# Performance work log

Measured on AMD Instinct MI355X. Metric: run time of the kernel, lower is better.

The kernel has to match this reference:

```python
import jax, jax.numpy as jnp
import numpy as np

B, N = 8192, 32          # batch of (user,item) pairs, AOS triples per pair
D1, D2 = 64, 64          # user/item and aspect/opinion embedding dims
H, O = 128, 64           # hidden_dims = [128, 64]
R = 3                    # n_relations (sentiments)
SLOPE = 0.01             # nn.LeakyReLU default negative_slope


def leaky_relu(x):
    return jnp.where(x >= 0, x, SLOPE * x)


def setup_inputs() -> dict:
    key = jax.random.key(0)
    ks = jax.random.split(key, 14)
    p = 0.1  # param scale
    return {
        "u_emb": jax.random.normal(ks[0], (B, D1), jnp.float32),
        "i_emb": jax.random.normal(ks[1], (B, D1), jnp.float32),
        "a_emb": jax.random.normal(ks[2], (B, N, D2), jnp.float32),
        "o_emb": jax.random.normal(ks[3], (B, N, D2), jnp.float32),
        "s": jax.random.randint(ks[4], (B, N), 0, R, jnp.int64),
        # per-relation AO MLP: Linear(128->128) + LeakyReLU, Linear(128->64) + LeakyReLU
        "ao_W0": jax.random.normal(ks[5], (R, 2 * D2, H), jnp.float32) * p,
        "ao_b0": jax.random.normal(ks[6], (R, H), jnp.float32) * p,
        "ao_W1": jax.random.normal(ks[7], (R, H, O), jnp.float32) * p,
        "ao_b1": jax.random.normal(ks[8], (R, O), jnp.float32) * p,
        # shared UI MLP: Linear(128->128) + LeakyReLU, Linear(128->64) + LeakyReLU
        "ui_W0": jax.random.normal(ks[9], (2 * D1, H), jnp.float32) * p,
        "ui_b0": jax.random.normal(ks[10], (H,), jnp.float32) * p,
        "ui_W1": jax.random.normal(ks[11], (H, O), jnp.float32) * p,
        "ui_b1": jax.random.normal(ks[12], (O,), jnp.float32) * p,
    }


def reference(u_emb, i_emb, a_emb, o_emb, s,
              ao_W0, ao_b0, ao_W1, ao_b1,
              ui_W0, ui_b0, ui_W1, ui_b1):
    # ui branch (shared MLP)
    ui_in = jnp.concatenate([u_emb, i_emb], axis=-1)            # [B, 2*D1]
    ui = leaky_relu(ui_in @ ui_W0 + ui_b0)                       # [B, H]
    ui = leaky_relu(ui @ ui_W1 + ui_b1)                          # [B, O]

    # ao branch: relation-specific MLPs. Instead of masked gather/scatter,
    # compute all R (small) relation MLPs densely and select per element.
    ao_in = jnp.concatenate([a_emb, o_emb], axis=-1)             # [B, N, 2*D2]
    h = leaky_relu(jnp.einsum('bnd,rdh->rbnh', ao_in, ao_W0)
                   + ao_b0[:, None, None, :])                    # [R, B, N, H]
    h = leaky_relu(jnp.einsum('rbnh,rho->rbno', h, ao_W1)
                   + ao_b1[:, None, None, :])                    # [R, B, N, O]

    h = jnp.moveaxis(h, 0, 2)                                    # [B, N, R, O]
    aos = jnp.take_along_axis(h, s[:, :, None, None], axis=2)[:, :, 0, :]  # [B, N, O]

    # loss == 'bpr': dot product score
    pred = jnp.sum(ui[:, None, :] * aos, axis=-1)                # [B, N]
    return pred
```

## Files before the change

kernel.cpp:

```cpp
#include <hip/hip_runtime.h>

typedef unsigned short u16t;
typedef __bf16 bf16x8 __attribute__((ext_vector_type(8)));
typedef float  f32x4  __attribute__((ext_vector_type(4)));

#define SLOPE 0.01f
#define SAP 136
#define UIP 72

__device__ __forceinline__ float lrelu(float x) { return x >= 0.0f ? x : SLOPE * x; }
__device__ __forceinline__ u16t f2b(float f) {
    union { float f; unsigned i; } x; x.f = f;
    return (u16t)((x.i + 0x7fffu + ((x.i >> 16) & 1u)) >> 16);
}
__device__ __forceinline__ float b2f(u16t u) {
    union { unsigned i; float f; } x; x.i = ((unsigned)u) << 16; return x.f;
}
__device__ __forceinline__ unsigned pk2(float a, float b) {
    unsigned r;
    asm("v_cvt_pk_bf16_f32 %0, %1, %2" : "=v"(r) : "v"(a), "v"(b));
    return r;
}
__device__ __forceinline__ uint4 pack8(float4 x, float4 y) {
    uint4 r; r.x = pk2(x.x, x.y); r.y = pk2(x.z, x.w);
    r.z = pk2(y.x, y.y); r.w = pk2(y.z, y.w); return r;
}
__device__ __forceinline__ int clmp3(int v) { return v < 0 ? 0 : (v > 2 ? 2 : v); }

__global__ __launch_bounds__(256) void kernelA(
    const float* __restrict__ W0, const float* __restrict__ W1,
    const float* __restrict__ uW0, const float* __restrict__ uW1,
    const int* __restrict__ s,
    u16t* __restrict__ W0p, u16t* __restrict__ W1p,
    u16t* __restrict__ U0p, u16t* __restrict__ U1p,
    int* __restrict__ cntB)
{
    __shared__ int sc[3];
    const int t = threadIdx.x;
    if (blockIdx.x < 384) {
        int tid = blockIdx.x * 256 + t;
        if (tid < 49152) {
            int j = tid & 7, lane = (tid >> 3) & 63, c = (tid >> 9) & 7,
                kk = (tid >> 12) & 3, r = tid >> 14;
            int k = kk * 32 + (lane >> 4) * 8 + j, n = c * 16 + (lane & 15);
            W0p[tid] = f2b(W0[(r * 128 + k) * 128 + n]);
        } else if (tid < 73728) {
            int t2 = tid - 49152;
            int j = t2 & 7, lane = (t2 >> 3) & 63, c = (t2 >> 9) & 3,
                kk = (t2 >> 11) & 3, r = t2 >> 13;
            int k = kk * 32 + (lane >> 4) * 8 + j, n = c * 16 + (lane & 15);
            W1p[t2] = f2b(W1[(r * 128 + k) * 64 + n]);
        } else if (tid < 90112) {
            int t3 = tid - 73728;
            int j = t3 & 7, lane = (t3 >> 3) & 63, c = (t3 >> 9) & 7, kk = t3 >> 12;
            int k = kk * 32 + (lane >> 4) * 8 + j, n = c * 16 + (lane & 15);
            U0p[t3] = f2b(uW0[k * 128 + n]);
        } else if (tid < 98304) {
            int t4 = tid - 90112;
            int j = t4 & 7, lane = (t4 >> 3) & 63, c = (t4 >> 9) & 3, kk = t4 >> 11;
            int k = kk * 32 + (lane >> 4) * 8 + j, n = c * 16 + (lane & 15);
            U1p[t4] = f2b(uW1[k * 64 + n]);
        }
    } else {
        const int blk = blockIdx.x - 384;
        if (t < 3) sc[t] = 0;
        __syncthreads();
        int4 sv = ((const int4*)s)[blk * 256 + t];
        int l0 = 0, l1 = 0, l2 = 0, r;
        r = clmp3(sv.x); l0 += (r == 0); l1 += (r == 1); l2 += (r == 2);
        r = clmp3(sv.y); l0 += (r == 0); l1 += (r == 1); l2 += (r == 2);
        r = clmp3(sv.z); l0 += (r == 0); l1 += (r == 1); l2 += (r == 2);
        r = clmp3(sv.w); l0 += (r == 0); l1 += (r == 1); l2 += (r == 2);
        atomicAdd(&sc[0], l0); atomicAdd(&sc[1], l1); atomicAdd(&sc[2], l2);
        __syncthreads();
        if (t < 3) cntB[blk * 3 + t] = sc[t];
    }
}

__global__ __launch_bounds__(512) void kernelB(
    const float* __restrict__ u_emb, const float* __restrict__ i_emb,
    const u16t* __restrict__ U0p, const u16t* __restrict__ U1p,
    const float* __restrict__ uib0, const float* __restrict__ uib1,
    const int* __restrict__ s, const int* __restrict__ cntB,
    u16t* __restrict__ uiT, int* __restrict__ cntOut, int* __restrict__ rows)
{
    __shared__ __align__(16) u16t sA[32 * SAP];
    __shared__ __align__(16) u16t sH[32 * SAP];
    __shared__ int sTab[768];
    __shared__ int sBT[6];
    __shared__ int sS[256];
    const int t = threadIdx.x;

    if (blockIdx.x < 256) {
        const int wave = t >> 6, lane = t & 63, m = lane & 15, kg = lane >> 4;
        const int c = wave, c2 = wave & 3, hlf = wave >> 2;
        const int B0 = blockIdx.x * 32;

        bf16x8 w0f[4], w1f[4];
#pragma unroll
        for (int kk = 0; kk < 4; ++kk) {
            w0f[kk] = *(const bf16x8*)(U0p + (((kk * 8 + c) * 64 + lane) << 3));
            w1f[kk] = *(const bf16x8*)(U1p + (((kk * 4 + c2) * 64 + lane) << 3));
        }
        const float b0 = uib0[c * 16 + m], b1 = uib1[c2 * 16 + m];

        {
            const int row = t >> 4, seg = t & 15;
            const float* src = (seg < 8) ? (u_emb + (size_t)(B0 + row) * 64 + seg * 8)
                                         : (i_emb + (size_t)(B0 + row) * 64 + (seg - 8) * 8);
            float4 v0 = ((const float4*)src)[0], v1 = ((const float4*)src)[1];
            *(uint4*)&sA[row * SAP + seg * 8] = pack8(v0, v1);
        }
        __syncthreads();

#pragma unroll
        for (int mt = 0; mt < 2; ++mt) {
            const u16t* ap = &sA[(mt * 16 + m) * SAP + kg * 8];
            bf16x8 a0 = *(const bf16x8*)(ap),      a1 = *(const bf16x8*)(ap + 32);
            bf16x8 a2 = *(const bf16x8*)(ap + 64), a3 = *(const bf16x8*)(ap + 96);
            f32x4 acc = {0.f, 0.f, 0.f, 0.f};
            acc = __builtin_amdgcn_mfma_f32_16x16x32_bf16(a0, w0f[0], acc, 0, 0, 0);
            acc = __builtin_amdgcn_mfma_f32_16x16x32_bf16(a1, w0f[1], acc, 0, 0, 0);
            acc = __builtin_amdgcn_mfma_f32_16x16x32_bf16(a2, w0f[2], acc, 0, 0, 0);
            acc = __builtin_amdgcn_mfma_f32_16x16x32_bf16(a3, w0f[3], acc, 0, 0, 0);
#pragma unroll
            for (int j = 0; j < 4; ++j)
                sH[(mt * 16 + kg * 4 + j) * SAP + c * 16 + m] = f2b(lrelu(acc[j] + b0));
        }
        __syncthreads();

        {
            const int mt = hlf;
            const u16t* hp = &sH[(mt * 16 + m) * SAP + kg * 8];
            bf16x8 a0 = *(const bf16x8*)(hp),      a1 = *(const bf16x8*)(hp + 32);
            bf16x8 a2 = *(const bf16x8*)(hp + 64), a3 = *(const bf16x8*)(hp + 96);
            f32x4 acc = {0.f, 0.f, 0.f, 0.f};
            acc = __builtin_amdgcn_mfma_f32_16x16x32_bf16(a0, w1f[0], acc, 0, 0, 0);
            acc = __builtin_amdgcn_mfma_f32_16x16x32_bf16(a1, w1f[1], acc, 0, 0, 0);
            acc = __builtin_amdgcn_mfma_f32_16x16x32_bf16(a2, w1f[2], acc, 0, 0, 0);
            acc = __builtin_amdgcn_mfma_f32_16x16x32_bf16(a3, w1f[3], acc, 0, 0, 0);
#pragma unroll
            for (int j = 0; j < 4; ++j)
                uiT[(size_t)(B0 + mt * 16 + kg * 4 + j) * 64 + c2 * 16 + m] =
                    f2b(lrelu(acc[j] + b1));
        }
    } else {
        const int blk = blockIdx.x - 256;
        if (t < 256) {
            sTab[t] = cntB[t]; sTab[t + 256] = cntB[t + 256]; sTab[t + 512] = cntB[t + 512];
        }
        __syncthreads();
        if (t < 3) {
            int base = 0, tot = 0;
            for (int b = 0; b < 256; ++b) {
                int v = sTab[b * 3 + t];
                if (b < blk) base += v;
                tot += v;
            }
            sBT[t] = base; sBT[3 + t] = tot;
        }
        int rr0 = 0, rr1 = 0, rr2 = 0, rr3 = 0, packed = 0;
        if (t < 256) {
            int4 sv = ((const int4*)s)[blk * 256 + t];
            rr0 = clmp3(sv.x); rr1 = clmp3(sv.y); rr2 = clmp3(sv.z); rr3 = clmp3(sv.w);
            packed = (1 << (11 * rr0)) + (1 << (11 * rr1))
                   + (1 << (11 * rr2)) + (1 << (11 * rr3));
            sS[t] = packed;
        }
        __syncthreads();
        for (int off = 1; off < 256; off <<= 1) {
            int v = 0;
            if (t >= off && t < 256) v = sS[t - off];
            __syncthreads();
            if (t < 256) sS[t] += v;
            __syncthreads();
        }
        if (t < 256) {
            const int excl = sS[t] - packed;
            const int g1 = sBT[3], g2 = sBT[3] + sBT[4];
            int rr[4] = { rr0, rr1, rr2, rr3 };
            int seen[3] = {0, 0, 0};
#pragma unroll
            for (int i = 0; i < 4; ++i) {
                int rl = rr[i];
                int gb = rl == 0 ? 0 : (rl == 1 ? g1 : g2);
                int pos = gb + sBT[rl] + ((excl >> (11 * rl)) & 2047) + seen[rl];
                seen[rl]++;
                rows[pos] = blk * 1024 + t * 4 + i;
            }
        }
        if (blk == 0 && t < 3) cntOut[t] = sBT[3 + t];
    }
}

__global__ __launch_bounds__(512, 4) void ao_main(
    const float* __restrict__ a_emb, const float* __restrict__ o_emb,
    const float* __restrict__ ao_b0, const float* __restrict__ ao_b1,
    const u16t* __restrict__ W0p, const u16t* __restrict__ W1p,
    const u16t* __restrict__ uiT, const int* __restrict__ rows,
    const int* __restrict__ tot, float* __restrict__ out)
{
    __shared__ __align__(16) u16t sA[64 * SAP];
    __shared__ __align__(16) u16t sH[64 * SAP];
    __shared__ __align__(16) u16t sUIl[64 * UIP];
    __shared__ float sPred[64];

    const int n0 = tot[0], n1 = tot[1], n2 = tot[2];
    const int ch0 = (n0 + 63) >> 6, ch1 = (n1 + 63) >> 6, ch2 = (n2 + 63) >> 6;
    const int nch = ch0 + ch1 + ch2;

    const int t = threadIdx.x, wave = t >> 6, lane = t & 63, m = lane & 15, kg = lane >> 4;
    const int c = wave, c2 = wave & 3, hlf = wave >> 2;

    bf16x8 w0f[4], w1f[4];
    float b0 = 0.f, b1 = 0.f;
    int rprev = -1;

    for (int ci = 0; ci < 2; ++ci) {
        const int chunk = blockIdx.x * 2 + ci;
        if (chunk >= nch) break;
        int r, rel, bb, nb;
        if (chunk < ch0)            { r = 0; rel = chunk;             bb = 0;       nb = n0; }
        else if (chunk < ch0 + ch1) { r = 1; rel = chunk - ch0;       bb = n0;      nb = n1; }
        else                        { r = 2; rel = chunk - ch0 - ch1; bb = n0 + n1; nb = n2; }
        const int rstart = rel * 64;
        int nrows = nb - rstart; if (nrows > 64) nrows = 64;

        if (r != rprev) {
            const u16t* wp0 = W0p + r * 16384;
            const u16t* wp1 = W1p + r * 8192;
#pragma unroll
            for (int kk = 0; kk < 4; ++kk) {
                w0f[kk] = *(const bf16x8*)(wp0 + (((kk * 8 + c) * 64 + lane) << 3));
                w1f[kk] = *(const bf16x8*)(wp1 + (((kk * 4 + c2) * 64 + lane) << 3));
            }
            b0 = ao_b0[r * 128 + c * 16 + m];
            b1 = ao_b1[r * 64 + c2 * 16 + m];
            rprev = r;
        }

        {
            const int q = t >> 3, seg = t & 7;
            const int rid = rows[bb + rstart + (q < nrows ? q : nrows - 1)];
            const float* src = (seg < 4) ? (a_emb + (size_t)rid * 64 + seg * 16)
                                         : (o_emb + (size_t)rid * 64 + (seg - 4) * 16);
            float4 v0 = ((const float4*)src)[0], v1 = ((const float4*)src)[1];
            float4 v2 = ((const float4*)src)[2], v3 = ((const float4*)src)[3];
            uint4* dst = (uint4*)&sA[q * SAP + seg * 16];
            dst[0] = pack8(v0, v1);
            dst[1] = pack8(v2, v3);
            *(uint4*)&sUIl[q * UIP + seg * 8] =
                *(const uint4*)(uiT + ((size_t)(rid >> 5)) * 64 + seg * 8);
        }
        if (t < 64) sPred[t] = 0.0f;
        __syncthreads();

#pragma unroll
        for (int mt = 0; mt < 4; ++mt) {
            const u16t* ap = &sA[(mt * 16 + m) * SAP + kg * 8];
            bf16x8 a0 = *(const bf16x8*)(ap),      a1 = *(const bf16x8*)(ap + 32);
            bf16x8 a2 = *(const bf16x8*)(ap + 64), a3 = *(const bf16x8*)(ap + 96);
            f32x4 acc_a = {0.f, 0.f, 0.f, 0.f}, acc_b = {0.f, 0.f, 0.f, 0.f};
            acc_a = __builtin_amdgcn_mfma_f32_16x16x32_bf16(a0, w0f[0], acc_a, 0, 0, 0);
            acc_a = __builtin_amdgcn_mfma_f32_16x16x32_bf16(a1, w0f[1], acc_a, 0, 0, 0);
            acc_b = __builtin_amdgcn_mfma_f32_16x16x32_bf16(a2, w0f[2], acc_b, 0, 0, 0);
            acc_b = __builtin_amdgcn_mfma_f32_16x16x32_bf16(a3, w0f[3], acc_b, 0, 0, 0);
            f32x4 acc = acc_a + acc_b;
#pragma unroll
            for (int j = 0; j < 4; ++j)
                sH[(mt * 16 + kg * 4 + j) * SAP + c * 16 + m] = f2b(lrelu(acc[j] + b0));
        }
        __syncthreads();

        for (int mt = hlf; mt < 4; mt += 2) {
            const u16t* hp = &sH[(mt * 16 + m) * SAP + kg * 8];
            bf16x8 a0 = *(const bf16x8*)(hp),      a1 = *(const bf16x8*)(hp + 32);
            bf16x8 a2 = *(const bf16x8*)(hp + 64), a3 = *(const bf16x8*)(hp + 96);
            f32x4 acc_a = {0.f, 0.f, 0.f, 0.f}, acc_b = {0.f, 0.f, 0.f, 0.f};
            acc_a = __builtin_amdgcn_mfma_f32_16x16x32_bf16(a0, w1f[0], acc_a, 0, 0, 0);
            acc_a = __builtin_amdgcn_mfma_f32_16x16x32_bf16(a1, w1f[1], acc_a, 0, 0, 0);
            acc_b = __builtin_amdgcn_mfma_f32_16x16x32_bf16(a2, w1f[2], acc_b, 0, 0, 0);
            acc_b = __builtin_amdgcn_mfma_f32_16x16x32_bf16(a3, w1f[3], acc_b, 0, 0, 0);
            f32x4 acc = acc_a + acc_b;
            const int o = c2 * 16 + m;
            float pj[4];
#pragma unroll
            for (int j = 0; j < 4; ++j) {
                const int q = mt * 16 + kg * 4 + j;
                pj[j] = lrelu(acc[j] + b1) * b2f(sUIl[q * UIP + o]);
            }
#pragma unroll
            for (int msk = 8; msk >= 1; msk >>= 1) {
#pragma unroll
                for (int j = 0; j < 4; ++j) pj[j] += __shfl_xor(pj[j], msk, 16);
            }
            if (m == 0) {
#pragma unroll
                for (int j = 0; j < 4; ++j)
                    atomicAdd(&sPred[mt * 16 + kg * 4 + j], pj[j]);
            }
        }
        __syncthreads();

        if (t < nrows) out[rows[bb + rstart + t]] = sPred[t];
    }
}

extern "C" void kernel_launch(void* const* d_in, const int* in_sizes, int n_in,
                              void* d_out, int out_size, void* d_ws, size_t ws_size,
                              hipStream_t stream) {
    (void)in_sizes; (void)n_in; (void)out_size; (void)ws_size;
    const float* u_emb = (const float*)d_in[0];
    const float* i_emb = (const float*)d_in[1];
    const float* a_emb = (const float*)d_in[2];
    const float* o_emb = (const float*)d_in[3];
    const int*   s     = (const int*)  d_in[4];
    const float* aoW0  = (const float*)d_in[5];
    const float* aob0  = (const float*)d_in[6];
    const float* aoW1  = (const float*)d_in[7];
    const float* aob1  = (const float*)d_in[8];
    const float* uiW0  = (const float*)d_in[9];
    const float* uib0  = (const float*)d_in[10];
    const float* uiW1  = (const float*)d_in[11];
    const float* uib1  = (const float*)d_in[12];
    float* out = (float*)d_out;

    char* ws = (char*)d_ws;
    u16t* W0p  = (u16t*)(ws);
    u16t* W1p  = (u16t*)(ws + 98304);
    u16t* U0p  = (u16t*)(ws + 147456);
    u16t* U1p  = (u16t*)(ws + 180224);
    u16t* uiT  = (u16t*)(ws + 196608);
    int*  cntB = (int*) (ws + 1245184);
    int*  totC = (int*) (ws + 1248256);
    int*  rowsP= (int*) (ws + 1248272);

    kernelA<<<dim3(640), dim3(256), 0, stream>>>(
        aoW0, aoW1, uiW0, uiW1, s, W0p, W1p, U0p, U1p, cntB);
    kernelB<<<dim3(512), dim3(512), 0, stream>>>(
        u_emb, i_emb, U0p, U1p, uib0, uib1, s, cntB, uiT, totC, rowsP);
    ao_main<<<dim3(2051), dim3(512), 0, stream>>>(
        a_emb, o_emb, aob0, aob1, W0p, W1p, uiT, rowsP, totC, out);
}
```

Before: 199.9 us.

## Software-pipeline gathers across chunks with double-buffered UI tiles and fewer barriers

The ao_main kernel now handles four 64-row chunks per block instead of two, and the grid is halved. While the current chunk's MFMAs run, it prefetches the next chunk's a/o embeddings and UI vectors into registers and looks up row indices two chunks ahead. The UI tile and prediction buffers are double-buffered, and each output write is deferred to the following iteration, which cuts the barriers per chunk from three to two. This is meant to hide global gather latency behind compute, at the cost of more register pressure and fewer blocks to balance load across the GPU.

```diff
diff --git a/kernel.cpp b/kernel.cpp
--- a/kernel.cpp
+++ b/kernel.cpp
@@ -7,6 +7,7 @@
 #define SLOPE 0.01f
 #define SAP 136
 #define UIP 72
+#define CPB 4
 
 __device__ __forceinline__ float lrelu(float x) { return x >= 0.0f ? x : SLOPE * x; }
 __device__ __forceinline__ u16t f2b(float f) {
@@ -26,6 +27,12 @@
     r.z = pk2(y.x, y.y); r.w = pk2(y.z, y.w); return r;
 }
 __device__ __forceinline__ int clmp3(int v) { return v < 0 ? 0 : (v > 2 ? 2 : v); }
+
+__device__ __forceinline__ void block_sync() {
+    asm volatile("s_waitcnt lgkmcnt(0)" ::: "memory");
+    __builtin_amdgcn_s_barrier();
+    asm volatile("" ::: "memory");
+}
 
 __global__ __launch_bounds__(256) void kernelA(
     const float* __restrict__ W0, const float* __restrict__ W1,
@@ -193,6 +200,18 @@
     }
 }
 
+__device__ __forceinline__ void chunk_info(int chunk, int ch0, int ch01,
+                                           int n0, int n1, int n2,
+                                           int& r, int& bb, int& rstart, int& nrows)
+{
+    int rel, nb;
+    if (chunk < ch0)       { r = 0; rel = chunk;        bb = 0;       nb = n0; }
+    else if (chunk < ch01) { r = 1; rel = chunk - ch0;  bb = n0;      nb = n1; }
+    else                   { r = 2; rel = chunk - ch01; bb = n0 + n1; nb = n2; }
+    rstart = rel * 64;
+    int nr = nb - rstart; nrows = nr > 64 ? 64 : nr;
+}
+
 __global__ __launch_bounds__(512, 4) void ao_main(
     const float* __restrict__ a_emb, const float* __restrict__ o_emb,
     const float* __restrict__ ao_b0, const float* __restrict__ ao_b1,
@@ -202,29 +221,55 @@
 {
     __shared__ __align__(16) u16t sA[64 * SAP];
     __shared__ __align__(16) u16t sH[64 * SAP];
-    __shared__ __align__(16) u16t sUIl[64 * UIP];
-    __shared__ float sPred[64];
+    __shared__ __align__(16) u16t sUIl[2][64 * UIP];
+    __shared__ float sPred[2][64];
 
     const int n0 = tot[0], n1 = tot[1], n2 = tot[2];
     const int ch0 = (n0 + 63) >> 6, ch1 = (n1 + 63) >> 6, ch2 = (n2 + 63) >> 6;
-    const int nch = ch0 + ch1 + ch2;
+    const int ch01 = ch0 + ch1;
+    const int nch = ch01 + ch2;
+    const int chunk0 = blockIdx.x * CPB;
+    if (chunk0 >= nch) return;
 
     const int t = threadIdx.x, wave = t >> 6, lane = t & 63, m = lane & 15, kg = lane >> 4;
     const int c = wave, c2 = wave & 3, hlf = wave >> 2;
+    const int q = t >> 3, seg = t & 7;
 
     bf16x8 w0f[4], w1f[4];
     float b0 = 0.f, b1 = 0.f;
     int rprev = -1;
 
-    for (int ci = 0; ci < 2; ++ci) {
-        const int chunk = blockIdx.x * 2 + ci;
+    int r0, bb0, rs0, nr0;
+    chunk_info(chunk0, ch0, ch01, n0, n1, n2, r0, bb0, rs0, nr0);
+    int ridCur = rows[bb0 + rs0 + (q < nr0 ? q : nr0 - 1)];
+
+    float4 pv0, pv1, pv2, pv3; uint4 puv;
+    {
+        const float* src = (seg < 4) ? (a_emb + (size_t)ridCur * 64 + seg * 16)
+                                     : (o_emb + (size_t)ridCur * 64 + (seg - 4) * 16);
+        pv0 = ((const float4*)src)[0]; pv1 = ((const float4*)src)[1];
+        pv2 = ((const float4*)src)[2]; pv3 = ((const float4*)src)[3];
+        puv = *(const uint4*)(uiT + ((size_t)(ridCur >> 5)) * 64 + seg * 8);
+    }
+    int ridNext = 0;
+    if (CPB > 1 && chunk0 + 1 < nch) {
+        int r1, bb1, rs1, nr1;
+        chunk_info(chunk0 + 1, ch0, ch01, n0, n1, n2, r1, bb1, rs1, nr1);
+        ridNext = rows[bb1 + rs1 + (q < nr1 ? q : nr1 - 1)];
+    }
+    {
+        uint4* dst = (uint4*)&sA[q * SAP + seg * 16];
+        dst[0] = pack8(pv0, pv1); dst[1] = pack8(pv2, pv3);
+        *(uint4*)&sUIl[0][q * UIP + seg * 8] = puv;
+    }
+    int ridPrev = 0, nrowsPrev = 0, lastPar = 0;
+    block_sync();
+
+    for (int ci = 0; ci < CPB; ++ci) {
+        const int chunk = chunk0 + ci;
         if (chunk >= nch) break;
-        int r, rel, bb, nb;
-        if (chunk < ch0)            { r = 0; rel = chunk;             bb = 0;       nb = n0; }
-        else if (chunk < ch0 + ch1) { r = 1; rel = chunk - ch0;       bb = n0;      nb = n1; }
-        else                        { r = 2; rel = chunk - ch0 - ch1; bb = n0 + n1; nb = n2; }
-        const int rstart = rel * 64;
-        int nrows = nb - rstart; if (nrows > 64) nrows = 64;
+        int r, bb, rstart, nrows;
+        chunk_info(chunk, ch0, ch01, n0, n1, n2, r, bb, rstart, nrows);
 
         if (r != rprev) {
             const u16t* wp0 = W0p + r * 16384;
@@ -239,21 +284,24 @@
             rprev = r;
         }
 
-        {
-            const int q = t >> 3, seg = t & 7;
-            const int rid = rows[bb + rstart + (q < nrows ? q : nrows - 1)];
-            const float* src = (seg < 4) ? (a_emb + (size_t)rid * 64 + seg * 16)
-                                         : (o_emb + (size_t)rid * 64 + (seg - 4) * 16);
-            float4 v0 = ((const float4*)src)[0], v1 = ((const float4*)src)[1];
-            float4 v2 = ((const float4*)src)[2], v3 = ((const float4*)src)[3];
-            uint4* dst = (uint4*)&sA[q * SAP + seg * 16];
-            dst[0] = pack8(v0, v1);
-            dst[1] = pack8(v2, v3);
-            *(uint4*)&sUIl[q * UIP + seg * 8] =
-                *(const uint4*)(uiT + ((size_t)(rid >> 5)) * 64 + seg * 8);
-        }
-        if (t < 64) sPred[t] = 0.0f;
-        __syncthreads();
+        const bool valid1 = (ci + 1 < CPB) && (chunk + 1 < nch);
+        const bool valid2 = (ci + 2 < CPB) && (chunk + 2 < nch);
+        if (valid1) {
+            const float* src = (seg < 4) ? (a_emb + (size_t)ridNext * 64 + seg * 16)
+                                         : (o_emb + (size_t)ridNext * 64 + (seg - 4) * 16);
+            pv0 = ((const float4*)src)[0]; pv1 = ((const float4*)src)[1];
+            pv2 = ((const float4*)src)[2]; pv3 = ((const float4*)src)[3];
+            puv = *(const uint4*)(uiT + ((size_t)(ridNext >> 5)) * 64 + seg * 8);
+        }
+        int ridNext2 = 0;
+        if (valid2) {
+            int r2, bb2, rs2, nr2;
+            chunk_info(chunk + 2, ch0, ch01, n0, n1, n2, r2, bb2, rs2, nr2);
+            ridNext2 = rows[bb2 + rs2 + (q < nr2 ? q : nr2 - 1)];
+        }
+        if (ci > 0 && seg == 0 && q < nrowsPrev)
+            out[ridPrev] = sPred[(ci - 1) & 1][q];
+        if (t < 64) sPred[ci & 1][t] = 0.0f;
 
 #pragma unroll
         for (int mt = 0; mt < 4; ++mt) {
@@ -266,16 +314,21 @@
             acc_b = __builtin_amdgcn_mfma_f32_16x16x32_bf16(a2, w0f[2], acc_b, 0, 0, 0);
             acc_b = __builtin_amdgcn_mfma_f32_16x16x32_bf16(a3, w0f[3], acc_b, 0, 0, 0);
             f32x4 acc = acc_a + acc_b;
-#pragma unroll
-            for (int j = 0; j < 4; ++j)
-                sH[(mt * 16 + kg * 4 + j) * SAP + c * 16 + m] = f2b(lrelu(acc[j] + b0));
-        }
-        __syncthreads();
-
+            unsigned pA = pk2(lrelu(acc[0] + b0), lrelu(acc[1] + b0));
+            unsigned pB = pk2(lrelu(acc[2] + b0), lrelu(acc[3] + b0));
+            u16t* hp = &sH[(mt * 16 + kg * 4) * SAP + c * 16 + m];
+            hp[0]       = (u16t)pA;
+            hp[SAP]     = (u16t)(pA >> 16);
+            hp[2 * SAP] = (u16t)pB;
+            hp[3 * SAP] = (u16t)(pB >> 16);
+        }
+        block_sync();
+
+        const int par = ci & 1;
         for (int mt = hlf; mt < 4; mt += 2) {
-            const u16t* hp = &sH[(mt * 16 + m) * SAP + kg * 8];
-            bf16x8 a0 = *(const bf16x8*)(hp),      a1 = *(const bf16x8*)(hp + 32);
-            bf16x8 a2 = *(const bf16x8*)(hp + 64), a3 = *(const bf16x8*)(hp + 96);
+            const u16t* hp2 = &sH[(mt * 16 + m) * SAP + kg * 8];
+            bf16x8 a0 = *(const bf16x8*)(hp2),      a1 = *(const bf16x8*)(hp2 + 32);
+            bf16x8 a2 = *(const bf16x8*)(hp2 + 64), a3 = *(const bf16x8*)(hp2 + 96);
             f32x4 acc_a = {0.f, 0.f, 0.f, 0.f}, acc_b = {0.f, 0.f, 0.f, 0.f};
             acc_a = __builtin_amdgcn_mfma_f32_16x16x32_bf16(a0, w1f[0], acc_a, 0, 0, 0);
             acc_a = __builtin_amdgcn_mfma_f32_16x16x32_bf16(a1, w1f[1], acc_a, 0, 0, 0);
@@ -286,8 +339,8 @@
             float pj[4];
 #pragma unroll
             for (int j = 0; j < 4; ++j) {
-                const int q = mt * 16 + kg * 4 + j;
-                pj[j] = lrelu(acc[j] + b1) * b2f(sUIl[q * UIP + o]);
+                const int rq = mt * 16 + kg * 4 + j;
+                pj[j] = lrelu(acc[j] + b1) * b2f(sUIl[par][rq * UIP + o]);
             }
 #pragma unroll
             for (int msk = 8; msk >= 1; msk >>= 1) {
@@ -297,13 +350,21 @@
             if (m == 0) {
 #pragma unroll
                 for (int j = 0; j < 4; ++j)
-                    atomicAdd(&sPred[mt * 16 + kg * 4 + j], pj[j]);
-            }
-        }
-        __syncthreads();
-
-        if (t < nrows) out[rows[bb + rstart + t]] = sPred[t];
-    }
+                    atomicAdd(&sPred[par][mt * 16 + kg * 4 + j], pj[j]);
+            }
+        }
+        if (valid1) {
+            uint4* dst = (uint4*)&sA[q * SAP + seg * 16];
+            dst[0] = pack8(pv0, pv1); dst[1] = pack8(pv2, pv3);
+            *(uint4*)&sUIl[par ^ 1][q * UIP + seg * 8] = puv;
+        }
+        ridPrev = ridCur; nrowsPrev = nrows; ridCur = ridNext; ridNext = ridNext2;
+        lastPar = par;
+        block_sync();
+    }
+
+    if (seg == 0 && q < nrowsPrev)
+        out[ridPrev] = sPred[lastPar][q];
 }
 
 extern "C" void kernel_launch(void* const* d_in, const int* in_sizes, int n_in,
@@ -339,6 +400,6 @@
         aoW0, aoW1, uiW0, uiW1, s, W0p, W1p, U0p, U1p, cntB);
     kernelB<<<dim3(512), dim3(512), 0, stream>>>(
         u_emb, i_emb, U0p, U1p, uib0, uib1, s, cntB, uiT, totC, rowsP);
-    ao_main<<<dim3(2051), dim3(512), 0, stream>>>(
+    ao_main<<<dim3(1025), dim3(512), 0, stream>>>(
         a_emb, o_emb, aob0, aob1, W0p, W1p, uiT, rowsP, totC, out);
 }
```

Result: slower. 204.2 us (+2.1%).
